# Kernel tuning notes

Measured on AMD Instinct MI355X. Metric: run time of the kernel, lower is better.

The kernel has to match this reference:

```python
import jax, jax.numpy as jnp
import numpy as np

B, C, H = 8, 768, 12
TH = TW = 16
SH = SW = 32
N = TH * TW + SH * SW  # 1280


def setup_inputs() -> dict:
    key = jax.random.key(0)
    k1, k2, k3 = jax.random.split(key, 3)
    return {
        "x": jax.random.normal(k1, (B, N, C), jnp.float32),
        "qkv_w": jax.random.normal(k2, (3 * C, C), jnp.float32) * 0.02,
        "proj_w": jax.random.normal(k3, (C, C), jnp.float32) * 0.02,
        "proj_b": jnp.zeros((C,), jnp.float32),
        "t_h": TH, "t_w": TW, "s_h": SH, "s_w": SW,
    }


def reference(x, qkv_w, proj_w, proj_b, t_h, t_w, s_h, s_w):
    Bb, Nn, Cc = x.shape
    hd = Cc // H
    scale = hd ** -0.5
    nt = t_h * t_w
    ns = s_h * s_w
    # qkv projection: torch Linear computes x @ W.T
    qkv = (x @ qkv_w.T).reshape(Bb, Nn, 3, H, hd).transpose(2, 0, 3, 1, 4)
    q, k, v = qkv[0], qkv[1], qkv[2]  # each [B, H, N, hd]
    q_mt, q_s = q[:, :, :nt], q[:, :, nt:]
    k_mt, v_mt = k[:, :, :nt], v[:, :, :nt]
    # template queries attend only to template keys
    attn_t = jax.nn.softmax(jnp.einsum('bhqd,bhkd->bhqk', q_mt, k_mt) * scale, axis=-1)
    x_mt = jnp.einsum('bhqk,bhkd->bhqd', attn_t, v_mt).transpose(0, 2, 1, 3).reshape(Bb, nt, Cc)
    # search queries attend to all (template + search) keys
    attn_s = jax.nn.softmax(jnp.einsum('bhqd,bhkd->bhqk', q_s, k) * scale, axis=-1)
    x_s = jnp.einsum('bhqk,bhkd->bhqd', attn_s, v).transpose(0, 2, 1, 3).reshape(Bb, ns, Cc)
    out = jnp.concatenate([x_mt, x_s], axis=1)
    out = out @ proj_w.T + proj_b
    return out
```

## Files before the change

### kernel.cpp

```cpp
#include <hip/hip_runtime.h>
#include <hip/hip_bf16.h>


typedef __attribute__((ext_vector_type(8))) short s8v;
typedef __attribute__((ext_vector_type(4))) float f4v;
typedef __attribute__((ext_vector_type(4))) unsigned short u4v;
typedef __attribute__((ext_vector_type(4))) unsigned int u4i;
typedef __attribute__((ext_vector_type(2))) unsigned int u2i;

#define MFMA16(a, b, c) __builtin_amdgcn_mfma_f32_16x16x32_bf16((a), (b), (c), 0, 0, 0)

#define QSCALE 0.1803368801f

__device__ __forceinline__ unsigned short f2bf(float f) {
  unsigned int u = __builtin_bit_cast(unsigned int, f);
  u += 0x7fffu + ((u >> 16) & 1u);
  return (unsigned short)(u >> 16);
}

__device__ __forceinline__ unsigned int pk2(float lo, float hi) {
  __hip_bfloat162 t = __float22bfloat162_rn(make_float2(lo, hi));
  unsigned int u;
  __builtin_memcpy(&u, &t, 4);
  return u;
}

__device__ __forceinline__ s8v pack8(const float* p0, const float* p1) {
  u4i pi;
  pi[0] = pk2(p0[0], p0[1]);
  pi[1] = pk2(p0[2], p0[3]);
  pi[2] = pk2(p1[0], p1[1]);
  pi[3] = pk2(p1[2], p1[3]);
  return __builtin_bit_cast(s8v, pi);
}

__global__ __launch_bounds__(256) void cvt3_kernel(const float* __restrict__ x,
                                                   const float* __restrict__ wq,
                                                   const float* __restrict__ wp,
                                                   unsigned short* __restrict__ xb,
                                                   unsigned short* __restrict__ wqb,
                                                   unsigned short* __restrict__ wpb) {
  int i = blockIdx.x * 256 + threadIdx.x;
  const float* src;
  unsigned short* dst;
  int j;
  if (i < 1966080) {
    src = x; dst = xb; j = i;
  } else if (i < 1966080 + 442368) {
    src = wq; dst = wqb; j = i - 1966080;
  } else {
    src = wp; dst = wpb; j = i - (1966080 + 442368);
  }
  f4v v = ((const f4v*)src)[j];
  u4v o;
  o[0] = f2bf(v[0]); o[1] = f2bf(v[1]); o[2] = f2bf(v[2]); o[3] = f2bf(v[3]);
  ((u4v*)dst)[j] = o;
}


#define GEMM_STAGE(AS, BS, kt_)                                                             \
  do {                                                                                      \
    __builtin_amdgcn_global_load_lds(                                                       \
        (const __attribute__((address_space(1))) unsigned int*)(gA0 + (kt_)),               \
        (__attribute__((address_space(3))) unsigned int*)((char*)(AS) + tid * 16), 16, 0, 0); \
    __builtin_amdgcn_global_load_lds(                                                       \
        (const __attribute__((address_space(1))) unsigned int*)(gB0 + (kt_)),               \
        (__attribute__((address_space(3))) unsigned int*)((char*)(BS) + tid * 16), 16, 0, 0); \
    __builtin_amdgcn_global_load_lds(                                                       \
        (const __attribute__((address_space(1))) unsigned int*)(gA1 + (kt_)),               \
        (__attribute__((address_space(3))) unsigned int*)((char*)(AS) + (256 + tid) * 16),  \
        16, 0, 0);                                                                          \
    __builtin_amdgcn_global_load_lds(                                                       \
        (const __attribute__((address_space(1))) unsigned int*)(gB1 + (kt_)),               \
        (__attribute__((address_space(3))) unsigned int*)((char*)(BS) + (256 + tid) * 16),  \
        16, 0, 0);                                                                          \
  } while (0)

#define PIPE_WAIT(cond_more)                                                                \
  do {                                                                                      \
    if (cond_more) asm volatile("s_waitcnt vmcnt(4) lgkmcnt(0)" ::: "memory");              \
    else           asm volatile("s_waitcnt vmcnt(0) lgkmcnt(0)" ::: "memory");              \
    __builtin_amdgcn_s_barrier();                                                           \
    __builtin_amdgcn_sched_barrier(0);                                                      \
  } while (0)

__global__ __launch_bounds__(256) void gemm_qkv_kernel(
    const unsigned short* __restrict__ A,
    const unsigned short* __restrict__ Bm,
    unsigned short* __restrict__ qb, unsigned short* __restrict__ kb,
    unsigned short* __restrict__ vT) {
  const int K = 768;
  __shared__ __align__(16) unsigned short As[3][128 * 32];
  __shared__ __align__(16) unsigned short Bs[3][128 * 32];
  int tid = threadIdx.x;
  int wave = tid >> 6, lane = tid & 63;
  int quad = lane >> 4, l16 = lane & 15;
  int wm = wave >> 1, wn = wave & 1;
  int l = blockIdx.x;
  int xcd = l & 7;
  int idx = l >> 3;
  int by = xcd * 10 + idx / 18;
  int bxg = idx - (idx / 18) * 18;
  int m0 = by * 128, n0 = bxg * 128;

  int srow = tid >> 2, scol = (tid & 3) << 3;
  const unsigned short* gA0 = A + (size_t)(m0 + srow) * K + scol;
  const unsigned short* gA1 = A + (size_t)(m0 + srow + 64) * K + scol;
  const unsigned short* gB0 = Bm + (size_t)(n0 + srow) * K + scol;
  const unsigned short* gB1 = Bm + (size_t)(n0 + srow + 64) * K + scol;

  f4v acc[4][4];
#pragma unroll
  for (int i = 0; i < 4; ++i)
#pragma unroll
    for (int j = 0; j < 4; ++j) acc[i][j] = (f4v){0.f, 0.f, 0.f, 0.f};

  GEMM_STAGE(As[0], Bs[0], 0);
  GEMM_STAGE(As[1], Bs[1], 32);

  int bfc = 0, bfs = 2;
  for (int t = 0; t < 24; ++t) {
    PIPE_WAIT(t + 1 < 24);
    if (t + 2 < 24) GEMM_STAGE(As[bfs], Bs[bfs], (t + 2) * 32);

    const unsigned short* Ab = As[bfc];
    const unsigned short* Bb = Bs[bfc];
    s8v af[4], bfr[4];
#pragma unroll
    for (int mi = 0; mi < 4; ++mi)
      af[mi] = *(const s8v*)&Ab[(wm * 64 + mi * 16 + l16) * 32 + quad * 8];
#pragma unroll
    for (int ni = 0; ni < 4; ++ni)
      bfr[ni] = *(const s8v*)&Bb[(wn * 64 + ni * 16 + l16) * 32 + quad * 8];
#pragma unroll
    for (int mi = 0; mi < 4; ++mi)
#pragma unroll
      for (int ni = 0; ni < 4; ++ni)
        acc[mi][ni] = MFMA16(af[mi], bfr[ni], acc[mi][ni]);

    bfc = (bfc == 2) ? 0 : bfc + 1;
    bfs = (bfs == 2) ? 0 : bfs + 1;
  }

  int which = n0 / 768;
  if (which == 2) {
#pragma unroll
    for (int ni = 0; ni < 4; ++ni) {
      int oo = n0 + wn * 64 + ni * 16 + l16 - 1536;
      int hh = oo >> 6;
      int dd = oo & 63;
#pragma unroll
      for (int mi = 0; mi < 4; ++mi) {
        int gm = m0 + wm * 64 + mi * 16 + quad * 4;
        int bb = gm / 1280;
        int nn = gm - bb * 1280;
        u2i w;
        w[0] = pk2(acc[mi][ni][0], acc[mi][ni][1]);
        w[1] = pk2(acc[mi][ni][2], acc[mi][ni][3]);
        *(u2i*)(vT + (((size_t)bb * 12 + hh) * 64 + dd) * 1280 + nn) = w;
      }
    }
  } else {
    unsigned short* dst = which ? kb : qb;
    float sc = which ? 1.0f : QSCALE;
#pragma unroll
    for (int ni = 0; ni < 4; ++ni) {
      int oo = n0 + wn * 64 + ni * 16 + l16 - which * 768;
      int hh = oo >> 6;
      int dd = oo & 63;
#pragma unroll
      for (int mi = 0; mi < 4; ++mi) {
#pragma unroll
        for (int r = 0; r < 4; ++r) {
          int gm = m0 + wm * 64 + mi * 16 + quad * 4 + r;
          int bb = gm / 1280;
          int nn = gm - bb * 1280;
          dst[(((size_t)bb * 12 + hh) * 1280 + nn) * 64 + dd] = f2bf(acc[mi][ni][r] * sc);
        }
      }
    }
  }
}

__global__ __launch_bounds__(256) void gemm_proj_kernel(
    const unsigned short* __restrict__ A,
    const unsigned short* __restrict__ Bm,
    const float* __restrict__ pb, float* __restrict__ out) {
  const int K = 768;
  __shared__ __align__(16) unsigned short As[3][128 * 32];
  __shared__ __align__(16) unsigned short Bs[3][128 * 32];
  int tid = threadIdx.x;
  int wave = tid >> 6, lane = tid & 63;
  int quad = lane >> 4, l16 = lane & 15;
  int wm = wave >> 1, wn = wave & 1;
  int l = blockIdx.x;
  int xcd = l & 7;
  int idx = l >> 3;
  int by = xcd * 10 + idx / 6;
  int bxg = idx - (idx / 6) * 6;
  int m0 = by * 128, n0 = bxg * 128;

  int srow = tid >> 2, scol = (tid & 3) << 3;
  const unsigned short* gA0 = A + (size_t)(m0 + srow) * K + scol;
  const unsigned short* gA1 = A + (size_t)(m0 + srow + 64) * K + scol;
  const unsigned short* gB0 = Bm + (size_t)(n0 + srow) * K + scol;
  const unsigned short* gB1 = Bm + (size_t)(n0 + srow + 64) * K + scol;

  f4v acc[4][4];
#pragma unroll
  for (int i = 0; i < 4; ++i)
#pragma unroll
    for (int j = 0; j < 4; ++j) acc[i][j] = (f4v){0.f, 0.f, 0.f, 0.f};

  GEMM_STAGE(As[0], Bs[0], 0);
  GEMM_STAGE(As[1], Bs[1], 32);

  int bfc = 0, bfs = 2;
  for (int t = 0; t < 24; ++t) {
    PIPE_WAIT(t + 1 < 24);
    if (t + 2 < 24) GEMM_STAGE(As[bfs], Bs[bfs], (t + 2) * 32);

    const unsigned short* Ab = As[bfc];
    const unsigned short* Bb = Bs[bfc];
    s8v af[4], bfr[4];
#pragma unroll
    for (int mi = 0; mi < 4; ++mi)
      af[mi] = *(const s8v*)&Ab[(wm * 64 + mi * 16 + l16) * 32 + quad * 8];
#pragma unroll
    for (int ni = 0; ni < 4; ++ni)
      bfr[ni] = *(const s8v*)&Bb[(wn * 64 + ni * 16 + l16) * 32 + quad * 8];
#pragma unroll
    for (int mi = 0; mi < 4; ++mi)
#pragma unroll
      for (int ni = 0; ni < 4; ++ni)
        acc[mi][ni] = MFMA16(af[mi], bfr[ni], acc[mi][ni]);

    bfc = (bfc == 2) ? 0 : bfc + 1;
    bfs = (bfs == 2) ? 0 : bfs + 1;
  }

#pragma unroll
  for (int ni = 0; ni < 4; ++ni) {
    int gn = n0 + wn * 64 + ni * 16 + l16;
    float bias = pb[gn];
#pragma unroll
    for (int mi = 0; mi < 4; ++mi)
#pragma unroll
      for (int r = 0; r < 4; ++r) {
        int gm = m0 + wm * 64 + mi * 16 + quad * 4 + r;
        out[(size_t)gm * 768 + gn] = acc[mi][ni][r] + bias;
      }
  }
}

__global__ __launch_bounds__(256) void attn_kernel(
    const unsigned short* __restrict__ qb, const unsigned short* __restrict__ kb,
    const unsigned short* __restrict__ vT, unsigned short* __restrict__ attnb) {
  const int NT = 1280, CC = 768;
  int l = blockIdx.x;
  int xcd = l & 7;
  int idx = l >> 3;
  int grp = xcd * 12 + idx / 10;
  int bx = idx - (idx / 10) * 10;
  int b = grp / 12;
  int h = grp - b * 12;
  int nk, qstart;
  if (bx < 8) { nk = 1280; qstart = 256 + bx * 128; }
  else        { nk = 256;  qstart = (bx - 8) * 128; }
  int wave = threadIdx.x >> 6, lane = threadIdx.x & 63;
  int quad = lane >> 4, l16 = lane & 15;
  int qa = qstart + wave * 32;
  int ntiles = nk >> 6;

  const unsigned short* qp = qb + (((size_t)b * 12 + h) * NT + qa) * 64;
  const unsigned short* kp = kb + (((size_t)b * 12 + h) * NT) * 64;
  const unsigned short* vp = vT + (((size_t)b * 12 + h) * 64) * NT;

  __shared__ __align__(16) unsigned short Kl[3][8][512];
  __shared__ __align__(16) unsigned short Vl[3][8][512];

  s8v bq0 = *(const s8v*)(qp + l16 * 64 + quad * 8);
  s8v bq1 = *(const s8v*)(qp + l16 * 64 + 32 + quad * 8);
  s8v bq2 = *(const s8v*)(qp + (16 + l16) * 64 + quad * 8);
  s8v bq3 = *(const s8v*)(qp + (16 + l16) * 64 + 32 + quad * 8);

  int perm = ((l16 >> 2) << 3) + (l16 & 3);
  int f0 = wave * 2, f1 = wave * 2 + 1;
  int koffs0, koffs1, voffs0, voffs1;
  {
    int s = f0 >> 2, dh = (f0 >> 1) & 1, hh = f0 & 1;
    koffs0 = (s * 32 + hh * 4 + perm) * 64 + (dh * 4 + quad) * 8;
    s = f1 >> 2; dh = (f1 >> 1) & 1; hh = f1 & 1;
    koffs1 = (s * 32 + hh * 4 + perm) * 64 + (dh * 4 + quad) * 8;
    int dt = f0 >> 1, sv = f0 & 1;
    voffs0 = (dt * 16 + l16) * NT + sv * 32 + quad * 8;
    dt = f1 >> 1; sv = f1 & 1;
    voffs1 = (dt * 16 + l16) * NT + sv * 32 + quad * 8;
  }

#define STAGE(bfi, k0_)                                                                     \
  do {                                                                                      \
    __builtin_amdgcn_global_load_lds(                                                       \
        (const __attribute__((address_space(1))) unsigned int*)(kp + (size_t)(k0_)*64 +     \
                                                                koffs0),                    \
        (__attribute__((address_space(3))) unsigned int*)((char*)&Kl[bfi][f0][0] +          \
                                                          lane * 16),                       \
        16, 0, 0);                                                                          \
    __builtin_amdgcn_global_load_lds(                                                       \
        (const __attribute__((address_space(1))) unsigned int*)(kp + (size_t)(k0_)*64 +     \
                                                                koffs1),                    \
        (__attribute__((address_space(3))) unsigned int*)((char*)&Kl[bfi][f1][0] +          \
                                                          lane * 16),                       \
        16, 0, 0);                                                                          \
    __builtin_amdgcn_global_load_lds(                                                       \
        (const __attribute__((address_space(1))) unsigned int*)(vp + (size_t)(k0_) +        \
                                                                voffs0),                    \
        (__attribute__((address_space(3))) unsigned int*)((char*)&Vl[bfi][f0][0] +          \
                                                          lane * 16),                       \
        16, 0, 0);                                                                          \
    __builtin_amdgcn_global_load_lds(                                                       \
        (const __attribute__((address_space(1))) unsigned int*)(vp + (size_t)(k0_) +        \
                                                                voffs1),                    \
        (__attribute__((address_space(3))) unsigned int*)((char*)&Vl[bfi][f1][0] +          \
                                                          lane * 16),                       \
        16, 0, 0);                                                                          \
  } while (0)

  float la = 0.f, lb = 0.f;
  f4v Oa[4], Ob[4];
#pragma unroll
  for (int dt = 0; dt < 4; ++dt) {
    Oa[dt] = (f4v){0.f, 0.f, 0.f, 0.f};
    Ob[dt] = (f4v){0.f, 0.f, 0.f, 0.f};
  }

  STAGE(0, 0);
  STAGE(1, 64);

  int bfc = 0, bfs = 2;
  for (int t = 0; t < ntiles; ++t) {
    PIPE_WAIT(t + 1 < ntiles);
    if (t + 2 < ntiles) STAGE(bfs, (t + 2) * 64);

    s8v kf[8], vf[8];
#pragma unroll
    for (int f = 0; f < 8; ++f) kf[f] = *(const s8v*)&Kl[bfc][f][lane * 8];
#pragma unroll
    for (int g = 0; g < 8; ++g) vf[g] = *(const s8v*)&Vl[bfc][g][lane * 8];

#pragma unroll
    for (int s = 0; s < 2; ++s) {
      int s4 = s << 2;
      f4v s0a = {0.f, 0.f, 0.f, 0.f}, s1a = {0.f, 0.f, 0.f, 0.f};
      f4v s0b = {0.f, 0.f, 0.f, 0.f}, s1b = {0.f, 0.f, 0.f, 0.f};
      s0a = MFMA16(kf[s4 | 0], bq0, s0a);
      s0a = MFMA16(kf[s4 | 2], bq1, s0a);
      s1a = MFMA16(kf[s4 | 1], bq0, s1a);
      s1a = MFMA16(kf[s4 | 3], bq1, s1a);
      s0b = MFMA16(kf[s4 | 0], bq2, s0b);
      s0b = MFMA16(kf[s4 | 2], bq3, s0b);
      s1b = MFMA16(kf[s4 | 1], bq2, s1b);
      s1b = MFMA16(kf[s4 | 3], bq3, s1b);

      float p0a[4], p1a[4], p0b[4], p1b[4];
#pragma unroll
      for (int r = 0; r < 4; ++r) {
        p0a[r] = __builtin_amdgcn_exp2f(s0a[r]);
        p1a[r] = __builtin_amdgcn_exp2f(s1a[r]);
        p0b[r] = __builtin_amdgcn_exp2f(s0b[r]);
        p1b[r] = __builtin_amdgcn_exp2f(s1b[r]);
      }
      la += ((p0a[0] + p0a[1]) + (p0a[2] + p0a[3])) + ((p1a[0] + p1a[1]) + (p1a[2] + p1a[3]));
      lb += ((p0b[0] + p0b[1]) + (p0b[2] + p0b[3])) + ((p1b[0] + p1b[1]) + (p1b[2] + p1b[3]));

      s8v pa = pack8(p0a, p1a);
      s8v pbv = pack8(p0b, p1b);

#pragma unroll
      for (int dt = 0; dt < 4; ++dt) {
        Oa[dt] = MFMA16(vf[dt * 2 + s], pa, Oa[dt]);
        Ob[dt] = MFMA16(vf[dt * 2 + s], pbv, Ob[dt]);
      }
    }

    bfc = (bfc == 2) ? 0 : bfc + 1;
    bfs = (bfs == 2) ? 0 : bfs + 1;
  }
#undef STAGE

  la += __shfl_xor(la, 16, 64);
  la += __shfl_xor(la, 32, 64);
  lb += __shfl_xor(lb, 16, 64);
  lb += __shfl_xor(lb, 32, 64);
  float inva = 1.f / la, invb = 1.f / lb;

  size_t rowa = ((size_t)b * NT + qa + l16) * CC + h * 64;
  size_t rowb = ((size_t)b * NT + qa + 16 + l16) * CC + h * 64;
#pragma unroll
  for (int dt = 0; dt < 4; ++dt) {
    u4v ova, ovb;
#pragma unroll
    for (int r = 0; r < 4; ++r) {
      ova[r] = f2bf(Oa[dt][r] * inva);
      ovb[r] = f2bf(Ob[dt][r] * invb);
    }
    *(u4v*)(attnb + rowa + dt * 16 + quad * 4) = ova;
    *(u4v*)(attnb + rowb + dt * 16 + quad * 4) = ovb;
  }
}

extern "C" void kernel_launch(void* const* d_in, const int* in_sizes, int n_in,
                              void* d_out, int out_size, void* d_ws, size_t ws_size,
                              hipStream_t stream) {
  const float* x = (const float*)d_in[0];
  const float* qkv_w = (const float*)d_in[1];
  const float* proj_w = (const float*)d_in[2];
  const float* proj_b = (const float*)d_in[3];
  float* out = (float*)d_out;

  char* ws = (char*)d_ws;
  unsigned short* xb = (unsigned short*)(ws + 0);
  unsigned short* wqkvb = (unsigned short*)(ws + 15728640);
  unsigned short* wpb = (unsigned short*)(ws + 19267584);
  unsigned short* qb = (unsigned short*)(ws + 20447232);
  unsigned short* kbuf = (unsigned short*)(ws + 36175872);
  unsigned short* vT = (unsigned short*)(ws + 51904512);
  unsigned short* attnb = xb;

  cvt3_kernel<<<dim3(9984), 256, 0, stream>>>(x, qkv_w, proj_w, xb, wqkvb, wpb);

  gemm_qkv_kernel<<<dim3(1440), 256, 0, stream>>>(xb, wqkvb, qb, kbuf, vT);
  attn_kernel<<<dim3(960), 256, 0, stream>>>(qb, kbuf, vT, attnb);
  gemm_proj_kernel<<<dim3(480), 256, 0, stream>>>(attnb, wpb, proj_b, out);
}
```

Before: 242.0 us.

## Use 8-wave attention blocks sharing K/V staging, with reordered MFMA/exp and setprio

The attention kernel now runs 512-thread blocks covering 256 queries, so each K/V tile staged into LDS is shared by eight waves instead of four. This halves the per-wave global-to-LDS loads and the block count. The inner loop is reordered: all QK^T MFMAs are issued up front with raised wave priority, and V fragments are loaded just before each PV half to reduce register pressure. Larger blocks may cause more tail imbalance between the long search blocks and the short template blocks, and the occupancy limit set by launch bounds may restrict registers.

```diff
diff --git a/kernel.cpp b/kernel.cpp
--- a/kernel.cpp
+++ b/kernel.cpp
@@ -76,9 +76,17 @@
         16, 0, 0);                                                                          \
   } while (0)
 
-#define PIPE_WAIT(cond_more)                                                                \
+#define PIPE_WAIT4(cond_more)                                                               \
   do {                                                                                      \
     if (cond_more) asm volatile("s_waitcnt vmcnt(4) lgkmcnt(0)" ::: "memory");              \
+    else           asm volatile("s_waitcnt vmcnt(0) lgkmcnt(0)" ::: "memory");              \
+    __builtin_amdgcn_s_barrier();                                                           \
+    __builtin_amdgcn_sched_barrier(0);                                                      \
+  } while (0)
+
+#define PIPE_WAIT2(cond_more)                                                               \
+  do {                                                                                      \
+    if (cond_more) asm volatile("s_waitcnt vmcnt(2) lgkmcnt(0)" ::: "memory");              \
     else           asm volatile("s_waitcnt vmcnt(0) lgkmcnt(0)" ::: "memory");              \
     __builtin_amdgcn_s_barrier();                                                           \
     __builtin_amdgcn_sched_barrier(0);                                                      \
@@ -120,7 +128,7 @@
 
   int bfc = 0, bfs = 2;
   for (int t = 0; t < 24; ++t) {
-    PIPE_WAIT(t + 1 < 24);
+    PIPE_WAIT4(t + 1 < 24);
     if (t + 2 < 24) GEMM_STAGE(As[bfs], Bs[bfs], (t + 2) * 32);
 
     const unsigned short* Ab = As[bfc];
@@ -217,7 +225,7 @@
 
   int bfc = 0, bfs = 2;
   for (int t = 0; t < 24; ++t) {
-    PIPE_WAIT(t + 1 < 24);
+    PIPE_WAIT4(t + 1 < 24);
     if (t + 2 < 24) GEMM_STAGE(As[bfs], Bs[bfs], (t + 2) * 32);
 
     const unsigned short* Ab = As[bfc];
@@ -253,20 +261,20 @@
   }
 }
 
-__global__ __launch_bounds__(256) void attn_kernel(
+__global__ __launch_bounds__(512, 6) void attn_kernel(
     const unsigned short* __restrict__ qb, const unsigned short* __restrict__ kb,
     const unsigned short* __restrict__ vT, unsigned short* __restrict__ attnb) {
   const int NT = 1280, CC = 768;
   int l = blockIdx.x;
   int xcd = l & 7;
   int idx = l >> 3;
-  int grp = xcd * 12 + idx / 10;
-  int bx = idx - (idx / 10) * 10;
+  int grp = xcd * 12 + idx / 5;
+  int bx = idx - (idx / 5) * 5;
   int b = grp / 12;
   int h = grp - b * 12;
   int nk, qstart;
-  if (bx < 8) { nk = 1280; qstart = 256 + bx * 128; }
-  else        { nk = 256;  qstart = (bx - 8) * 128; }
+  if (bx < 4) { nk = 1280; qstart = 256 + bx * 256; }
+  else        { nk = 256;  qstart = 0; }
   int wave = threadIdx.x >> 6, lane = threadIdx.x & 63;
   int quad = lane >> 4, l16 = lane & 15;
   int qa = qstart + wave * 32;
@@ -285,43 +293,22 @@
   s8v bq3 = *(const s8v*)(qp + (16 + l16) * 64 + 32 + quad * 8);
 
   int perm = ((l16 >> 2) << 3) + (l16 & 3);
-  int f0 = wave * 2, f1 = wave * 2 + 1;
-  int koffs0, koffs1, voffs0, voffs1;
-  {
-    int s = f0 >> 2, dh = (f0 >> 1) & 1, hh = f0 & 1;
-    koffs0 = (s * 32 + hh * 4 + perm) * 64 + (dh * 4 + quad) * 8;
-    s = f1 >> 2; dh = (f1 >> 1) & 1; hh = f1 & 1;
-    koffs1 = (s * 32 + hh * 4 + perm) * 64 + (dh * 4 + quad) * 8;
-    int dt = f0 >> 1, sv = f0 & 1;
-    voffs0 = (dt * 16 + l16) * NT + sv * 32 + quad * 8;
-    dt = f1 >> 1; sv = f1 & 1;
-    voffs1 = (dt * 16 + l16) * NT + sv * 32 + quad * 8;
-  }
+  int f = wave;
+  int koffs = ((f >> 2) * 32 + (f & 1) * 4 + perm) * 64 + (((f >> 1) & 1) * 4 + quad) * 8;
+  int voffs = ((f >> 1) * 16 + l16) * NT + (f & 1) * 32 + quad * 8;
 
 #define STAGE(bfi, k0_)                                                                     \
   do {                                                                                      \
     __builtin_amdgcn_global_load_lds(                                                       \
         (const __attribute__((address_space(1))) unsigned int*)(kp + (size_t)(k0_)*64 +     \
-                                                                koffs0),                    \
-        (__attribute__((address_space(3))) unsigned int*)((char*)&Kl[bfi][f0][0] +          \
+                                                                koffs),                     \
+        (__attribute__((address_space(3))) unsigned int*)((char*)&Kl[bfi][f][0] +           \
                                                           lane * 16),                       \
         16, 0, 0);                                                                          \
     __builtin_amdgcn_global_load_lds(                                                       \
-        (const __attribute__((address_space(1))) unsigned int*)(kp + (size_t)(k0_)*64 +     \
-                                                                koffs1),                    \
-        (__attribute__((address_space(3))) unsigned int*)((char*)&Kl[bfi][f1][0] +          \
-                                                          lane * 16),                       \
-        16, 0, 0);                                                                          \
-    __builtin_amdgcn_global_load_lds(                                                       \
         (const __attribute__((address_space(1))) unsigned int*)(vp + (size_t)(k0_) +        \
-                                                                voffs0),                    \
-        (__attribute__((address_space(3))) unsigned int*)((char*)&Vl[bfi][f0][0] +          \
-                                                          lane * 16),                       \
-        16, 0, 0);                                                                          \
-    __builtin_amdgcn_global_load_lds(                                                       \
-        (const __attribute__((address_space(1))) unsigned int*)(vp + (size_t)(k0_) +        \
-                                                                voffs1),                    \
-        (__attribute__((address_space(3))) unsigned int*)((char*)&Vl[bfi][f1][0] +          \
+                                                                voffs),                     \
+        (__attribute__((address_space(3))) unsigned int*)((char*)&Vl[bfi][f][0] +           \
                                                           lane * 16),                       \
         16, 0, 0);                                                                          \
   } while (0)
@@ -339,49 +326,74 @@
 
   int bfc = 0, bfs = 2;
   for (int t = 0; t < ntiles; ++t) {
-    PIPE_WAIT(t + 1 < ntiles);
+    PIPE_WAIT2(t + 1 < ntiles);
     if (t + 2 < ntiles) STAGE(bfs, (t + 2) * 64);
 
-    s8v kf[8], vf[8];
-#pragma unroll
-    for (int f = 0; f < 8; ++f) kf[f] = *(const s8v*)&Kl[bfc][f][lane * 8];
-#pragma unroll
-    for (int g = 0; g < 8; ++g) vf[g] = *(const s8v*)&Vl[bfc][g][lane * 8];
-
-#pragma unroll
-    for (int s = 0; s < 2; ++s) {
-      int s4 = s << 2;
-      f4v s0a = {0.f, 0.f, 0.f, 0.f}, s1a = {0.f, 0.f, 0.f, 0.f};
-      f4v s0b = {0.f, 0.f, 0.f, 0.f}, s1b = {0.f, 0.f, 0.f, 0.f};
-      s0a = MFMA16(kf[s4 | 0], bq0, s0a);
-      s0a = MFMA16(kf[s4 | 2], bq1, s0a);
-      s1a = MFMA16(kf[s4 | 1], bq0, s1a);
-      s1a = MFMA16(kf[s4 | 3], bq1, s1a);
-      s0b = MFMA16(kf[s4 | 0], bq2, s0b);
-      s0b = MFMA16(kf[s4 | 2], bq3, s0b);
-      s1b = MFMA16(kf[s4 | 1], bq2, s1b);
-      s1b = MFMA16(kf[s4 | 3], bq3, s1b);
-
-      float p0a[4], p1a[4], p0b[4], p1b[4];
-#pragma unroll
-      for (int r = 0; r < 4; ++r) {
-        p0a[r] = __builtin_amdgcn_exp2f(s0a[r]);
-        p1a[r] = __builtin_amdgcn_exp2f(s1a[r]);
-        p0b[r] = __builtin_amdgcn_exp2f(s0b[r]);
-        p1b[r] = __builtin_amdgcn_exp2f(s1b[r]);
-      }
-      la += ((p0a[0] + p0a[1]) + (p0a[2] + p0a[3])) + ((p1a[0] + p1a[1]) + (p1a[2] + p1a[3]));
-      lb += ((p0b[0] + p0b[1]) + (p0b[2] + p0b[3])) + ((p1b[0] + p1b[1]) + (p1b[2] + p1b[3]));
-
-      s8v pa = pack8(p0a, p1a);
-      s8v pbv = pack8(p0b, p1b);
-
-#pragma unroll
-      for (int dt = 0; dt < 4; ++dt) {
-        Oa[dt] = MFMA16(vf[dt * 2 + s], pa, Oa[dt]);
-        Ob[dt] = MFMA16(vf[dt * 2 + s], pbv, Ob[dt]);
-      }
-    }
+    s8v kf[8];
+#pragma unroll
+    for (int ff = 0; ff < 8; ++ff) kf[ff] = *(const s8v*)&Kl[bfc][ff][lane * 8];
+
+    f4v t0a = {0.f, 0.f, 0.f, 0.f}, t1a = {0.f, 0.f, 0.f, 0.f};
+    f4v t0b = {0.f, 0.f, 0.f, 0.f}, t1b = {0.f, 0.f, 0.f, 0.f};
+    f4v u0a = {0.f, 0.f, 0.f, 0.f}, u1a = {0.f, 0.f, 0.f, 0.f};
+    f4v u0b = {0.f, 0.f, 0.f, 0.f}, u1b = {0.f, 0.f, 0.f, 0.f};
+    __builtin_amdgcn_s_setprio(1);
+    t0a = MFMA16(kf[0], bq0, t0a); t0a = MFMA16(kf[2], bq1, t0a);
+    t1a = MFMA16(kf[1], bq0, t1a); t1a = MFMA16(kf[3], bq1, t1a);
+    t0b = MFMA16(kf[0], bq2, t0b); t0b = MFMA16(kf[2], bq3, t0b);
+    t1b = MFMA16(kf[1], bq2, t1b); t1b = MFMA16(kf[3], bq3, t1b);
+    u0a = MFMA16(kf[4], bq0, u0a); u0a = MFMA16(kf[6], bq1, u0a);
+    u1a = MFMA16(kf[5], bq0, u1a); u1a = MFMA16(kf[7], bq1, u1a);
+    u0b = MFMA16(kf[4], bq2, u0b); u0b = MFMA16(kf[6], bq3, u0b);
+    u1b = MFMA16(kf[5], bq2, u1b); u1b = MFMA16(kf[7], bq3, u1b);
+    __builtin_amdgcn_s_setprio(0);
+
+    float p0a[4], p1a[4], p0b[4], p1b[4];
+#pragma unroll
+    for (int r = 0; r < 4; ++r) {
+      p0a[r] = __builtin_amdgcn_exp2f(t0a[r]);
+      p1a[r] = __builtin_amdgcn_exp2f(t1a[r]);
+      p0b[r] = __builtin_amdgcn_exp2f(t0b[r]);
+      p1b[r] = __builtin_amdgcn_exp2f(t1b[r]);
+    }
+    la += ((p0a[0] + p0a[1]) + (p0a[2] + p0a[3])) + ((p1a[0] + p1a[1]) + (p1a[2] + p1a[3]));
+    lb += ((p0b[0] + p0b[1]) + (p0b[2] + p0b[3])) + ((p1b[0] + p1b[1]) + (p1b[2] + p1b[3]));
+    s8v pa0 = pack8(p0a, p1a);
+    s8v pb0 = pack8(p0b, p1b);
+
+    s8v vf0[4];
+#pragma unroll
+    for (int dt = 0; dt < 4; ++dt) vf0[dt] = *(const s8v*)&Vl[bfc][dt * 2][lane * 8];
+    __builtin_amdgcn_s_setprio(1);
+#pragma unroll
+    for (int dt = 0; dt < 4; ++dt) {
+      Oa[dt] = MFMA16(vf0[dt], pa0, Oa[dt]);
+      Ob[dt] = MFMA16(vf0[dt], pb0, Ob[dt]);
+    }
+    __builtin_amdgcn_s_setprio(0);
+
+#pragma unroll
+    for (int r = 0; r < 4; ++r) {
+      p0a[r] = __builtin_amdgcn_exp2f(u0a[r]);
+      p1a[r] = __builtin_amdgcn_exp2f(u1a[r]);
+      p0b[r] = __builtin_amdgcn_exp2f(u0b[r]);
+      p1b[r] = __builtin_amdgcn_exp2f(u1b[r]);
+    }
+    la += ((p0a[0] + p0a[1]) + (p0a[2] + p0a[3])) + ((p1a[0] + p1a[1]) + (p1a[2] + p1a[3]));
+    lb += ((p0b[0] + p0b[1]) + (p0b[2] + p0b[3])) + ((p1b[0] + p1b[1]) + (p1b[2] + p1b[3]));
+    s8v pa1 = pack8(p0a, p1a);
+    s8v pb1 = pack8(p0b, p1b);
+
+    s8v vf1[4];
+#pragma unroll
+    for (int dt = 0; dt < 4; ++dt) vf1[dt] = *(const s8v*)&Vl[bfc][dt * 2 + 1][lane * 8];
+    __builtin_amdgcn_s_setprio(1);
+#pragma unroll
+    for (int dt = 0; dt < 4; ++dt) {
+      Oa[dt] = MFMA16(vf1[dt], pa1, Oa[dt]);
+      Ob[dt] = MFMA16(vf1[dt], pb1, Ob[dt]);
+    }
+    __builtin_amdgcn_s_setprio(0);
 
     bfc = (bfc == 2) ? 0 : bfc + 1;
     bfs = (bfs == 2) ? 0 : bfs + 1;
@@ -430,6 +442,6 @@
   cvt3_kernel<<<dim3(9984), 256, 0, stream>>>(x, qkv_w, proj_w, xb, wqkvb, wpb);
 
   gemm_qkv_kernel<<<dim3(1440), 256, 0, stream>>>(xb, wqkvb, qb, kbuf, vT);
-  attn_kernel<<<dim3(960), 256, 0, stream>>>(qb, kbuf, vT, attnb);
+  attn_kernel<<<dim3(480), 512, 0, stream>>>(qb, kbuf, vT, attnb);
   gemm_proj_kernel<<<dim3(480), 256, 0, stream>>>(attnb, wpb, proj_b, out);
 }
```

Result: slower. 459.8 us (+90.0%).

## Swizzle GEMM LDS layout, add MFMA priority hints, and defer V fragment loads

Applied to the files above, without the earlier changes.

Both GEMM kernels now XOR-swizzle the 16-byte column chunk by row, both when staging global data into LDS and when reading it back, so fragment reads from shared memory hit fewer bank conflicts. The attention loop wraps its MFMA groups in s_setprio so waves issuing matrix ops are favoured, and it loads V fragments per sub-step rather than all up front, which lowers register pressure. The PIPE_WAIT macro is only renamed. The swizzle has to match exactly between the write and read sides, or the results are wrong.

```diff
diff --git a/kernel.cpp b/kernel.cpp
--- a/kernel.cpp
+++ b/kernel.cpp
@@ -76,7 +76,7 @@
         16, 0, 0);                                                                          \
   } while (0)
 
-#define PIPE_WAIT(cond_more)                                                                \
+#define PIPE_WAIT4(cond_more)                                                               \
   do {                                                                                      \
     if (cond_more) asm volatile("s_waitcnt vmcnt(4) lgkmcnt(0)" ::: "memory");              \
     else           asm volatile("s_waitcnt vmcnt(0) lgkmcnt(0)" ::: "memory");              \
@@ -103,12 +103,15 @@
   int bxg = idx - (idx / 18) * 18;
   int m0 = by * 128, n0 = bxg * 128;
 
-  int srow = tid >> 2, scol = (tid & 3) << 3;
+  int srow = tid >> 2;
+  int scol = (((tid & 3) ^ ((tid >> 3) & 3)) << 3);
   const unsigned short* gA0 = A + (size_t)(m0 + srow) * K + scol;
   const unsigned short* gA1 = A + (size_t)(m0 + srow + 64) * K + scol;
   const unsigned short* gB0 = Bm + (size_t)(n0 + srow) * K + scol;
   const unsigned short* gB1 = Bm + (size_t)(n0 + srow + 64) * K + scol;
 
+  int rquad = quad ^ ((l16 >> 1) & 3);
+
   f4v acc[4][4];
 #pragma unroll
   for (int i = 0; i < 4; ++i)
@@ -120,7 +123,7 @@
 
   int bfc = 0, bfs = 2;
   for (int t = 0; t < 24; ++t) {
-    PIPE_WAIT(t + 1 < 24);
+    PIPE_WAIT4(t + 1 < 24);
     if (t + 2 < 24) GEMM_STAGE(As[bfs], Bs[bfs], (t + 2) * 32);
 
     const unsigned short* Ab = As[bfc];
@@ -128,10 +131,10 @@
     s8v af[4], bfr[4];
 #pragma unroll
     for (int mi = 0; mi < 4; ++mi)
-      af[mi] = *(const s8v*)&Ab[(wm * 64 + mi * 16 + l16) * 32 + quad * 8];
+      af[mi] = *(const s8v*)&Ab[(wm * 64 + mi * 16 + l16) * 32 + rquad * 8];
 #pragma unroll
     for (int ni = 0; ni < 4; ++ni)
-      bfr[ni] = *(const s8v*)&Bb[(wn * 64 + ni * 16 + l16) * 32 + quad * 8];
+      bfr[ni] = *(const s8v*)&Bb[(wn * 64 + ni * 16 + l16) * 32 + rquad * 8];
 #pragma unroll
     for (int mi = 0; mi < 4; ++mi)
 #pragma unroll
@@ -200,12 +203,15 @@
   int bxg = idx - (idx / 6) * 6;
   int m0 = by * 128, n0 = bxg * 128;
 
-  int srow = tid >> 2, scol = (tid & 3) << 3;
+  int srow = tid >> 2;
+  int scol = (((tid & 3) ^ ((tid >> 3) & 3)) << 3);
   const unsigned short* gA0 = A + (size_t)(m0 + srow) * K + scol;
   const unsigned short* gA1 = A + (size_t)(m0 + srow + 64) * K + scol;
   const unsigned short* gB0 = Bm + (size_t)(n0 + srow) * K + scol;
   const unsigned short* gB1 = Bm + (size_t)(n0 + srow + 64) * K + scol;
 
+  int rquad = quad ^ ((l16 >> 1) & 3);
+
   f4v acc[4][4];
 #pragma unroll
   for (int i = 0; i < 4; ++i)
@@ -217,7 +223,7 @@
 
   int bfc = 0, bfs = 2;
   for (int t = 0; t < 24; ++t) {
-    PIPE_WAIT(t + 1 < 24);
+    PIPE_WAIT4(t + 1 < 24);
     if (t + 2 < 24) GEMM_STAGE(As[bfs], Bs[bfs], (t + 2) * 32);
 
     const unsigned short* Ab = As[bfc];
@@ -225,10 +231,10 @@
     s8v af[4], bfr[4];
 #pragma unroll
     for (int mi = 0; mi < 4; ++mi)
-      af[mi] = *(const s8v*)&Ab[(wm * 64 + mi * 16 + l16) * 32 + quad * 8];
+      af[mi] = *(const s8v*)&Ab[(wm * 64 + mi * 16 + l16) * 32 + rquad * 8];
 #pragma unroll
     for (int ni = 0; ni < 4; ++ni)
-      bfr[ni] = *(const s8v*)&Bb[(wn * 64 + ni * 16 + l16) * 32 + quad * 8];
+      bfr[ni] = *(const s8v*)&Bb[(wn * 64 + ni * 16 + l16) * 32 + rquad * 8];
 #pragma unroll
     for (int mi = 0; mi < 4; ++mi)
 #pragma unroll
@@ -339,20 +345,19 @@
 
   int bfc = 0, bfs = 2;
   for (int t = 0; t < ntiles; ++t) {
-    PIPE_WAIT(t + 1 < ntiles);
+    PIPE_WAIT4(t + 1 < ntiles);
     if (t + 2 < ntiles) STAGE(bfs, (t + 2) * 64);
 
-    s8v kf[8], vf[8];
-#pragma unroll
-    for (int f = 0; f < 8; ++f) kf[f] = *(const s8v*)&Kl[bfc][f][lane * 8];
-#pragma unroll
-    for (int g = 0; g < 8; ++g) vf[g] = *(const s8v*)&Vl[bfc][g][lane * 8];
+    s8v kf[8];
+#pragma unroll
+    for (int ff = 0; ff < 8; ++ff) kf[ff] = *(const s8v*)&Kl[bfc][ff][lane * 8];
 
 #pragma unroll
     for (int s = 0; s < 2; ++s) {
       int s4 = s << 2;
       f4v s0a = {0.f, 0.f, 0.f, 0.f}, s1a = {0.f, 0.f, 0.f, 0.f};
       f4v s0b = {0.f, 0.f, 0.f, 0.f}, s1b = {0.f, 0.f, 0.f, 0.f};
+      __builtin_amdgcn_s_setprio(1);
       s0a = MFMA16(kf[s4 | 0], bq0, s0a);
       s0a = MFMA16(kf[s4 | 2], bq1, s0a);
       s1a = MFMA16(kf[s4 | 1], bq0, s1a);
@@ -361,6 +366,7 @@
       s0b = MFMA16(kf[s4 | 2], bq3, s0b);
       s1b = MFMA16(kf[s4 | 1], bq2, s1b);
       s1b = MFMA16(kf[s4 | 3], bq3, s1b);
+      __builtin_amdgcn_s_setprio(0);
 
       float p0a[4], p1a[4], p0b[4], p1b[4];
 #pragma unroll
@@ -376,11 +382,16 @@
       s8v pa = pack8(p0a, p1a);
       s8v pbv = pack8(p0b, p1b);
 
+      s8v vf[4];
+#pragma unroll
+      for (int dt = 0; dt < 4; ++dt) vf[dt] = *(const s8v*)&Vl[bfc][dt * 2 + s][lane * 8];
+      __builtin_amdgcn_s_setprio(1);
 #pragma unroll
       for (int dt = 0; dt < 4; ++dt) {
-        Oa[dt] = MFMA16(vf[dt * 2 + s], pa, Oa[dt]);
-        Ob[dt] = MFMA16(vf[dt * 2 + s], pbv, Ob[dt]);
+        Oa[dt] = MFMA16(vf[dt], pa, Oa[dt]);
+        Ob[dt] = MFMA16(vf[dt], pbv, Ob[dt]);
       }
+      __builtin_amdgcn_s_setprio(0);
     }
 
     bfc = (bfc == 2) ? 0 : bfc + 1;
```

Measured after the change: 247.5 us. 1.02x slower.
